# Optimization experiments

Measured on AMD Instinct MI355X. Metric: run time of the kernel, lower is better.

Reference implementation:

```python
import jax, jax.numpy as jnp
import numpy as np

NUM_HEADS = 16
ROPE_BASE = 10000.0
LN_EPS = 1e-5


def _rope_tables(seq_len, head_dim, dtype):
    # half-dim angle table: (seq_len, head_dim//2)
    inv_freq = 1.0 / (ROPE_BASE ** (jnp.arange(0, head_dim, 2, dtype=jnp.float32) / head_dim))
    angles = jnp.arange(seq_len, dtype=jnp.float32)[:, None] * inv_freq[None, :]
    return jnp.cos(angles).astype(dtype), jnp.sin(angles).astype(dtype)


def _apply_rope(x, cos, sin):
    # x: (B, H, S, D_h); rotate interleaved (even, odd) dim pairs
    xe = x[..., 0::2]
    xo = x[..., 1::2]
    c = cos[None, None, :, :]
    s = sin[None, None, :, :]
    re = xe * c - xo * s
    ro = xe * s + xo * c
    return jnp.stack([re, ro], axis=-1).reshape(x.shape)


def _layernorm(x, g, b):
    mu = jnp.mean(x, axis=-1, keepdims=True)
    var = jnp.var(x, axis=-1, keepdims=True)
    return (x - mu) * jax.lax.rsqrt(var + LN_EPS) * g + b


def setup_inputs() -> dict:
    key = jax.random.key(0)
    ks = jax.random.split(key, 8)
    B, S, D, F = 2, 2048, 1024, 4096
    sd = lambda fan_in: 1.0 / np.sqrt(fan_in)
    return {
        "x": jax.random.normal(ks[0], (B, S, D), jnp.float32),
        "in_proj_w": jax.random.normal(ks[1], (3 * D, D), jnp.float32) * sd(D),
        "in_proj_b": jnp.zeros((3 * D,), jnp.float32),
        "out_w": jax.random.normal(ks[2], (D, D), jnp.float32) * sd(D),
        "out_b": jnp.zeros((D,), jnp.float32),
        "w1": jax.random.normal(ks[3], (F, D), jnp.float32) * sd(D),
        "b1": jnp.zeros((F,), jnp.float32),
        "w2": jax.random.normal(ks[4], (D, F), jnp.float32) * sd(F),
        "b2": jnp.zeros((D,), jnp.float32),
        "ln1_g": jnp.ones((D,), jnp.float32),
        "ln1_b": jnp.zeros((D,), jnp.float32),
        "ln2_g": jnp.ones((D,), jnp.float32),
        "ln2_b": jnp.zeros((D,), jnp.float32),
    }


def reference(x, in_proj_w, in_proj_b, out_w, out_b, w1, b1, w2, b2,
              ln1_g, ln1_b, ln2_g, ln2_b):
    B, S, D = x.shape
    H = NUM_HEADS
    Dh = D // H
    scale = Dh ** -0.5

    # fused QKV projection
    qkv = x @ in_proj_w.T + in_proj_b  # (B, S, 3D)
    q, k, v = jnp.split(qkv, 3, axis=-1)
    q = q.reshape(B, S, H, Dh).transpose(0, 2, 1, 3)
    k = k.reshape(B, S, H, Dh).transpose(0, 2, 1, 3)
    v = v.reshape(B, S, H, Dh).transpose(0, 2, 1, 3)

    cos, sin = _rope_tables(S, Dh, x.dtype)
    q = _apply_rope(q, cos, sin)
    k = _apply_rope(k, cos, sin)

    # SDPA (no mask, no dropout)
    scores = jnp.einsum('bhqd,bhkd->bhqk', q, k) * scale
    probs = jax.nn.softmax(scores, axis=-1)
    attn = jnp.einsum('bhqk,bhkd->bhqd', probs, v)
    attn = attn.transpose(0, 2, 1, 3).reshape(B, S, D)
    attn_out = attn @ out_w.T + out_b

    # post-norm encoder layer: residual + LN, FFN, residual + LN
    h = _layernorm(x + attn_out, ln1_g, ln1_b)
    ff = jax.nn.relu(h @ w1.T + b1) @ w2.T + b2
    return _layernorm(h + ff, ln2_g, ln2_b)
```

## Files before the change

### kernel.cpp

```cpp
#include <hip/hip_runtime.h>
#include <math.h>

typedef unsigned short u16;
typedef unsigned int u32;
typedef __attribute__((ext_vector_type(8))) __bf16 bf16x8;
typedef __attribute__((ext_vector_type(4))) float f32x4;

#define AS1 __attribute__((address_space(1)))
#define AS3 __attribute__((address_space(3)))

#define B_ 2
#define S_ 2048
#define D_ 1024
#define H_ 16
#define DH_ 64
#define F_ 4096
#define M_ 4096

__device__ __forceinline__ u16 f2b(float f) {
  u32 u = __builtin_bit_cast(u32, f);
  u += 0x7fffu + ((u >> 16) & 1u);
  return (u16)(u >> 16);
}

__global__ __launch_bounds__(256) void cvt_kernel(const float* __restrict__ in,
                                                  u16* __restrict__ out, int n4) {
  int i = blockIdx.x * 256 + threadIdx.x;
  if (i < n4) {
    float4 v = ((const float4*)in)[i];
    ushort4 o;
    o.x = f2b(v.x); o.y = f2b(v.y); o.z = f2b(v.z); o.w = f2b(v.w);
    ((ushort4*)out)[i] = o;
  }
}

__global__ __launch_bounds__(256) void tables_kernel(float* __restrict__ cosT,
                                                     float* __restrict__ sinT) {
  int idx = blockIdx.x * 256 + threadIdx.x;
  int s = idx >> 5, i = idx & 31;
  float inv = powf(10000.0f, -(float)i / 32.0f);
  float ang = (float)s * inv;
  cosT[idx] = cosf(ang);
  sinT[idx] = sinf(ang);
}

template <bool BIAS, bool RELU, bool RESID, typename OutT>
__global__ __launch_bounds__(256) void gemm_bt(const u16* __restrict__ A,
                                               const u16* __restrict__ Bm,
                                               const float* __restrict__ bias,
                                               const float* __restrict__ resid,
                                               OutT* __restrict__ C, int M, int N, int K) {
  __shared__ u16 sA[128 * 32];
  __shared__ u16 sB[128 * 32];
  const int t = threadIdx.x;
  const int w = t >> 6, lane = t & 63;
  const int fr = lane & 15, fg = lane >> 4;
  const int row0 = blockIdx.y * 128, col0 = blockIdx.x * 128;
  const int wr = (w >> 1) * 64, wc = (w & 1) * 64;

  f32x4 acc[4][4] = {};

  const int rA = t >> 2;
  const int cB = (t & 3) * 16;
  const char* aRead = (const char*)sA + (((wr + fr) * 32 + fg * 8) << 1);
  const char* bRead = (const char*)sB + (((wc + fr) * 32 + fg * 8) << 1);

  for (int k0 = 0; k0 < K; k0 += 32) {
#pragma unroll
    for (int i = 0; i < 2; ++i) {
      const char* srcA = (const char*)(A + (size_t)(row0 + i * 64 + rA) * K + k0) + cB;
      const char* srcB = (const char*)(Bm + (size_t)(col0 + i * 64 + rA) * K + k0) + cB;
      char* dA = (char*)sA + i * 4096 + w * 1024;
      char* dB = (char*)sB + i * 4096 + w * 1024;
      __builtin_amdgcn_global_load_lds((const AS1 u32*)srcA, (AS3 u32*)dA, 16, 0, 0);
      __builtin_amdgcn_global_load_lds((const AS1 u32*)srcB, (AS3 u32*)dB, 16, 0, 0);
    }
    __syncthreads();

    bf16x8 af[4], bfr[4];
#pragma unroll
    for (int m = 0; m < 4; ++m) af[m] = *(const bf16x8*)(aRead + m * 1024);
#pragma unroll
    for (int n = 0; n < 4; ++n) bfr[n] = *(const bf16x8*)(bRead + n * 1024);
#pragma unroll
    for (int m = 0; m < 4; ++m)
#pragma unroll
      for (int n = 0; n < 4; ++n)
        acc[m][n] = __builtin_amdgcn_mfma_f32_16x16x32_bf16(af[m], bfr[n], acc[m][n], 0, 0, 0);
    __syncthreads();
  }

#pragma unroll
  for (int m = 0; m < 4; ++m) {
    const int rowb = row0 + wr + m * 16 + fg * 4;
#pragma unroll
    for (int n = 0; n < 4; ++n) {
      const int col = col0 + wc + n * 16 + fr;
      float bv = BIAS ? bias[col] : 0.0f;
      f32x4 c = acc[m][n];
#pragma unroll
      for (int r = 0; r < 4; ++r) {
        float v = c[r] + bv;
        if (RESID) v += resid[(size_t)(rowb + r) * N + col];
        if (RELU) v = fmaxf(v, 0.0f);
        if constexpr (sizeof(OutT) == 2)
          ((u16*)C)[(size_t)(rowb + r) * N + col] = f2b(v);
        else
          ((float*)C)[(size_t)(rowb + r) * N + col] = v;
      }
    }
  }
}

__global__ __launch_bounds__(256) void rope_kernel(const float* __restrict__ qkv,
                                                   const float* __restrict__ cosT,
                                                   const float* __restrict__ sinT,
                                                   u16* __restrict__ qr, u16* __restrict__ kr,
                                                   u16* __restrict__ vt) {
  const int bh = blockIdx.x;
  const int b = bh >> 4, h = bh & 15;
  const int s0 = blockIdx.y * 64;
  const int t = threadIdx.x;

#pragma unroll
  for (int part = 0; part < 2; ++part) {
    const float* src = qkv + (size_t)(b * S_ + s0) * (3 * D_) + part * D_ + h * DH_;
    u16* dst = (part ? kr : qr) + ((size_t)bh * S_ + s0) * DH_;
    for (int it = 0; it < 8; ++it) {
      int item = it * 256 + t;
      int sl = item >> 5, i = item & 31;
      float2 x2 = *(const float2*)(src + (size_t)sl * (3 * D_) + 2 * i);
      int s = s0 + sl;
      float c = cosT[s * 32 + i], sn = sinT[s * 32 + i];
      float re = x2.x * c - x2.y * sn;
      float ro = x2.x * sn + x2.y * c;
      u32 packed = (u32)f2b(re) | ((u32)f2b(ro) << 16);
      *(u32*)(dst + (size_t)sl * DH_ + 2 * i) = packed;
    }
  }

  __shared__ float tile[64][65];
  const float* vsrc = qkv + (size_t)(b * S_ + s0) * (3 * D_) + 2 * D_ + h * DH_;
  for (int it = 0; it < 16; ++it) {
    int sl = it * 4 + (t >> 6), dh = t & 63;
    tile[sl][dh] = vsrc[(size_t)sl * (3 * D_) + dh];
  }
  __syncthreads();
  u16* vdst = vt + (size_t)bh * DH_ * S_ + s0;
  for (int it = 0; it < 16; ++it) {
    int dh = it * 4 + (t >> 6), sl = t & 63;
    vdst[(size_t)dh * S_ + sl] = f2b(tile[sl][dh]);
  }
}

__global__ __launch_bounds__(256) void attn_kernel(const u16* __restrict__ qr,
                                                   const u16* __restrict__ kr,
                                                   const u16* __restrict__ vt,
                                                   u16* __restrict__ attn) {
  __shared__ u16 sK[2][64 * 64];
  __shared__ u16 sV[2][64 * 64];
  __shared__ u16 plds[4][1024];
  const int bh = blockIdx.x;
  const int b = bh >> 4, h = bh & 15;
  const int q0 = blockIdx.y * 64;
  const int t = threadIdx.x, w = t >> 6, lane = t & 63;
  const int fr = lane & 15, fg = lane >> 4;

  const int qrow = q0 + w * 16 + fr;
  const u16* qbase = qr + ((size_t)bh * S_ + qrow) * DH_;
  bf16x8 qf0 = *(const bf16x8*)(qbase + fg * 8);
  bf16x8 qf1 = *(const bf16x8*)(qbase + 32 + fg * 8);

  const char* kByte = (const char*)(kr + (size_t)bh * S_ * DH_);
  const char* vByte = (const char*)(vt + (size_t)bh * DH_ * S_);
  char* pbase = (char*)&plds[w][0];
  const int ci0 = w * 64 + lane;

  f32x4 oacc[4] = {};
  float m_run = -1e30f, l_run = 0.0f;
  const float lscale = 0.125f * 1.44269504088896340736f;

  auto stage = [&](int bufb, int kt) {
#pragma unroll
    for (int i = 0; i < 2; ++i) {
      int ci = i * 256 + ci0;
      int r = ci >> 3, j = ci & 7;
      int jj = j ^ (r & 7);
      const char* srcK = kByte + (size_t)(kt + r) * 128 + (jj << 4);
      const char* srcV = vByte + (size_t)r * (S_ * 2) + (size_t)kt * 2 + (jj << 4);
      char* dK = (char*)&sK[bufb][0] + i * 4096 + w * 1024;
      char* dV = (char*)&sV[bufb][0] + i * 4096 + w * 1024;
      __builtin_amdgcn_global_load_lds((const AS1 u32*)srcK, (AS3 u32*)dK, 16, 0, 0);
      __builtin_amdgcn_global_load_lds((const AS1 u32*)srcV, (AS3 u32*)dV, 16, 0, 0);
    }
  };

  stage(0, 0);
  __syncthreads();

  int buf = 0;
  for (int kt = 0; kt < S_; kt += 64) {
    if (kt + 64 < S_) stage(buf ^ 1, kt + 64);

    const char* kB = (const char*)&sK[buf][0];
    const char* vB = (const char*)&sV[buf][0];

    f32x4 st[4];
#pragma unroll
    for (int ks = 0; ks < 4; ++ks) {
      const char* rowp = kB + (ks * 16 + fr) * 128;
      bf16x8 kf0 = *(const bf16x8*)(rowp + ((fg ^ (fr & 7)) << 4));
      bf16x8 kf1 = *(const bf16x8*)(rowp + (((fg + 4) ^ (fr & 7)) << 4));
      f32x4 z = {};
      z = __builtin_amdgcn_mfma_f32_16x16x32_bf16(kf0, qf0, z, 0, 0, 0);
      st[ks] = __builtin_amdgcn_mfma_f32_16x16x32_bf16(kf1, qf1, z, 0, 0, 0);
    }

    float pm = -1e30f;
#pragma unroll
    for (int ks = 0; ks < 4; ++ks) {
      st[ks] *= lscale;
#pragma unroll
      for (int r = 0; r < 4; ++r) pm = fmaxf(pm, st[ks][r]);
    }
    pm = fmaxf(pm, __shfl_xor(pm, 16));
    pm = fmaxf(pm, __shfl_xor(pm, 32));
    float mnew = fmaxf(m_run, pm);
    float alpha = __builtin_amdgcn_exp2f(m_run - mnew);
    float psum = 0.0f;
#pragma unroll
    for (int ks = 0; ks < 4; ++ks) {
      float p0 = __builtin_amdgcn_exp2f(st[ks][0] - mnew);
      float p1 = __builtin_amdgcn_exp2f(st[ks][1] - mnew);
      float p2 = __builtin_amdgcn_exp2f(st[ks][2] - mnew);
      float p3 = __builtin_amdgcn_exp2f(st[ks][3] - mnew);
      psum += (p0 + p1) + (p2 + p3);
      u32 lo = (u32)f2b(p0) | ((u32)f2b(p1) << 16);
      u32 hi = (u32)f2b(p2) | ((u32)f2b(p3) << 16);
      int wb = fr * 128 + (((ks * 32) | (fg * 8)) ^ ((fr & 7) << 4));
      *(uint2*)(pbase + wb) = make_uint2(lo, hi);
    }
    psum += __shfl_xor(psum, 16);
    psum += __shfl_xor(psum, 32);
    l_run = l_run * alpha + psum;
    m_run = mnew;
#pragma unroll
    for (int d = 0; d < 4; ++d) oacc[d] *= alpha;

    asm volatile("s_waitcnt lgkmcnt(0)" ::: "memory");
    __builtin_amdgcn_sched_barrier(0);

#pragma unroll
    for (int ksub = 0; ksub < 2; ++ksub) {
      int rb = fr * 128 + (((ksub * 64) | (fg * 16)) ^ ((fr & 7) << 4));
      bf16x8 pf = *(const bf16x8*)(pbase + rb);
#pragma unroll
      for (int d = 0; d < 4; ++d) {
        const char* vp = vB + (d * 16 + fr) * 128 + ((((ksub * 4) | fg) ^ (fr & 7)) << 4);
        bf16x8 vf = *(const bf16x8*)vp;
        oacc[d] = __builtin_amdgcn_mfma_f32_16x16x32_bf16(vf, pf, oacc[d], 0, 0, 0);
      }
    }
    __syncthreads();
    buf ^= 1;
  }

  const float inv_l = 1.0f / l_run;
  u16* obase = attn + (size_t)(b * S_ + q0 + w * 16 + fr) * D_ + h * DH_;
#pragma unroll
  for (int d = 0; d < 4; ++d) {
    ushort4 o4;
    o4.x = f2b(oacc[d][0] * inv_l);
    o4.y = f2b(oacc[d][1] * inv_l);
    o4.z = f2b(oacc[d][2] * inv_l);
    o4.w = f2b(oacc[d][3] * inv_l);
    *(ushort4*)(obase + d * 16 + fg * 4) = o4;
  }
}

template <bool WRITE_BF16>
__global__ __launch_bounds__(256) void ln_kernel(const float* __restrict__ in,
                                                 const float* __restrict__ gamma,
                                                 const float* __restrict__ beta,
                                                 float* __restrict__ outf,
                                                 u16* __restrict__ outb) {
  const int row = blockIdx.x;
  const int t = threadIdx.x;
  const float4 v = ((const float4*)(in + (size_t)row * D_))[t];
  float s = v.x + v.y + v.z + v.w;
  float ss = v.x * v.x + v.y * v.y + v.z * v.z + v.w * v.w;
#pragma unroll
  for (int off = 1; off < 64; off <<= 1) {
    s += __shfl_xor(s, off);
    ss += __shfl_xor(ss, off);
  }
  __shared__ float red[8];
  const int w = t >> 6, lane = t & 63;
  if (lane == 0) { red[w] = s; red[4 + w] = ss; }
  __syncthreads();
  s = red[0] + red[1] + red[2] + red[3];
  ss = red[4] + red[5] + red[6] + red[7];
  const float mu = s * (1.0f / D_);
  const float var = ss * (1.0f / D_) - mu * mu;
  const float rstd = rsqrtf(var + 1e-5f);
  const float4 g4 = ((const float4*)gamma)[t];
  const float4 b4 = ((const float4*)beta)[t];
  float4 o;
  o.x = (v.x - mu) * rstd * g4.x + b4.x;
  o.y = (v.y - mu) * rstd * g4.y + b4.y;
  o.z = (v.z - mu) * rstd * g4.z + b4.z;
  o.w = (v.w - mu) * rstd * g4.w + b4.w;
  ((float4*)(outf + (size_t)row * D_))[t] = o;
  if constexpr (WRITE_BF16) {
    ushort4 ob;
    ob.x = f2b(o.x); ob.y = f2b(o.y); ob.z = f2b(o.z); ob.w = f2b(o.w);
    ((ushort4*)(outb + (size_t)row * D_))[t] = ob;
  }
}

extern "C" void kernel_launch(void* const* d_in, const int* in_sizes, int n_in,
                              void* d_out, int out_size, void* d_ws, size_t ws_size,
                              hipStream_t stream) {
  const float* x = (const float*)d_in[0];
  const float* in_proj_w = (const float*)d_in[1];
  const float* in_proj_b = (const float*)d_in[2];
  const float* out_w = (const float*)d_in[3];
  const float* out_b = (const float*)d_in[4];
  const float* w1 = (const float*)d_in[5];
  const float* b1 = (const float*)d_in[6];
  const float* w2 = (const float*)d_in[7];
  const float* b2 = (const float*)d_in[8];
  const float* ln1_g = (const float*)d_in[9];
  const float* ln1_b = (const float*)d_in[10];
  const float* ln2_g = (const float*)d_in[11];
  const float* ln2_b = (const float*)d_in[12];

  char* ws = (char*)d_ws;
  u16* wib = (u16*)(ws + 0);
  u16* wob = (u16*)(ws + 6291456);
  u16* w1b = (u16*)(ws + 8388608);
  u16* w2b = (u16*)(ws + 16777216);
  float* cosT = (float*)(ws + 25165824);
  float* sinT = (float*)(ws + 25427968);
  float* qkv = (float*)(ws + 25690112);
  u16* ff = (u16*)(ws + 25690112);
  float* preln2 = (float*)(ws + 59244544);
  u16* xb = (u16*)(ws + 76021760);
  u16* attnb = (u16*)(ws + 76021760);
  u16* qrb = (u16*)(ws + 84410368);
  u16* krb = (u16*)(ws + 92798976);
  float* preln1 = (float*)(ws + 84410368);
  u16* vtb = (u16*)(ws + 101187584);
  u16* hb = (u16*)(ws + 101187584);
  float* hf = (float*)(ws + 109576192);
  (void)ws_size; (void)in_sizes; (void)n_in; (void)out_size;

  cvt_kernel<<<4096, 256, 0, stream>>>(x, xb, 1048576);
  cvt_kernel<<<3072, 256, 0, stream>>>(in_proj_w, wib, 786432);
  cvt_kernel<<<1024, 256, 0, stream>>>(out_w, wob, 262144);
  cvt_kernel<<<4096, 256, 0, stream>>>(w1, w1b, 1048576);
  cvt_kernel<<<4096, 256, 0, stream>>>(w2, w2b, 1048576);
  tables_kernel<<<256, 256, 0, stream>>>(cosT, sinT);

  gemm_bt<true, false, false, float><<<dim3(24, 32), 256, 0, stream>>>(
      xb, wib, in_proj_b, nullptr, qkv, M_, 3 * D_, D_);

  rope_kernel<<<dim3(32, 32), 256, 0, stream>>>(qkv, cosT, sinT, qrb, krb, vtb);

  attn_kernel<<<dim3(32, 32), 256, 0, stream>>>(qrb, krb, vtb, attnb);

  gemm_bt<true, false, true, float><<<dim3(8, 32), 256, 0, stream>>>(
      attnb, wob, out_b, x, preln1, M_, D_, D_);

  ln_kernel<true><<<4096, 256, 0, stream>>>(preln1, ln1_g, ln1_b, hf, hb);

  gemm_bt<true, true, false, u16><<<dim3(32, 32), 256, 0, stream>>>(
      hb, w1b, b1, nullptr, ff, M_, F_, D_);

  gemm_bt<true, false, true, float><<<dim3(8, 32), 256, 0, stream>>>(
      ff, w2b, b2, hf, preln2, M_, D_, F_);

  ln_kernel<false><<<4096, 256, 0, stream>>>(preln2, ln2_g, ln2_b, (float*)d_out, nullptr);
}
```

Before: 445.1 us.

## Split-K narrow GEMMs, fuse bias/residual into LN, swizzle LDS, bf16 QKV output

The N=1024 GEMMs (out-proj and FFN down) now use split-K across two z-slices writing fp32 partials, which doubles the block count from 256 to 512 to fill more CUs. A new reduce_ln kernel sums the partials with bias and residual before layernorm, replacing the separate residual epilogue. The GEMM LDS layout is XOR-swizzled to reduce bank conflicts on fragment reads. The QKV projection now writes bf16 instead of fp32, halving that traffic for the rope kernel. The cost is extra partial-buffer writes and reads, plus a small precision change on QKV.

```diff
diff --git a/kernel.cpp b/kernel.cpp
--- a/kernel.cpp
+++ b/kernel.cpp
@@ -44,12 +44,12 @@
   sinT[idx] = sinf(ang);
 }
 
-template <bool BIAS, bool RELU, bool RESID, typename OutT>
+template <bool BIAS, bool RELU, bool SPLIT, typename OutT>
 __global__ __launch_bounds__(256) void gemm_bt(const u16* __restrict__ A,
                                                const u16* __restrict__ Bm,
                                                const float* __restrict__ bias,
-                                               const float* __restrict__ resid,
-                                               OutT* __restrict__ C, int M, int N, int K) {
+                                               OutT* __restrict__ C, int M, int N, int K,
+                                               int kChunk) {
   __shared__ u16 sA[128 * 32];
   __shared__ u16 sB[128 * 32];
   const int t = threadIdx.x;
@@ -61,15 +61,17 @@
   f32x4 acc[4][4] = {};
 
   const int rA = t >> 2;
-  const int cB = (t & 3) * 16;
-  const char* aRead = (const char*)sA + (((wr + fr) * 32 + fg * 8) << 1);
-  const char* bRead = (const char*)sB + (((wc + fr) * 32 + fg * 8) << 1);
-
-  for (int k0 = 0; k0 < K; k0 += 32) {
+  const int jj = ((t & 3) ^ ((t >> 3) & 3)) << 4;
+  const int rdswz = ((fg ^ ((fr >> 1) & 3)) << 4);
+  const char* aRead = (const char*)sA + (wr + fr) * 64 + rdswz;
+  const char* bRead = (const char*)sB + (wc + fr) * 64 + rdswz;
+
+  const int kb = blockIdx.z * kChunk;
+  for (int k0 = kb; k0 < kb + kChunk; k0 += 32) {
 #pragma unroll
     for (int i = 0; i < 2; ++i) {
-      const char* srcA = (const char*)(A + (size_t)(row0 + i * 64 + rA) * K + k0) + cB;
-      const char* srcB = (const char*)(Bm + (size_t)(col0 + i * 64 + rA) * K + k0) + cB;
+      const char* srcA = (const char*)(A + (size_t)(row0 + i * 64 + rA) * K + k0) + jj;
+      const char* srcB = (const char*)(Bm + (size_t)(col0 + i * 64 + rA) * K + k0) + jj;
       char* dA = (char*)sA + i * 4096 + w * 1024;
       char* dB = (char*)sB + i * 4096 + w * 1024;
       __builtin_amdgcn_global_load_lds((const AS1 u32*)srcA, (AS3 u32*)dA, 16, 0, 0);
@@ -90,6 +92,8 @@
     __syncthreads();
   }
 
+  OutT* Cp = C;
+  if constexpr (SPLIT) Cp = C + (size_t)blockIdx.z * M * N;
 #pragma unroll
   for (int m = 0; m < 4; ++m) {
     const int rowb = row0 + wr + m * 16 + fg * 4;
@@ -101,18 +105,17 @@
 #pragma unroll
       for (int r = 0; r < 4; ++r) {
         float v = c[r] + bv;
-        if (RESID) v += resid[(size_t)(rowb + r) * N + col];
         if (RELU) v = fmaxf(v, 0.0f);
         if constexpr (sizeof(OutT) == 2)
-          ((u16*)C)[(size_t)(rowb + r) * N + col] = f2b(v);
+          ((u16*)Cp)[(size_t)(rowb + r) * N + col] = f2b(v);
         else
-          ((float*)C)[(size_t)(rowb + r) * N + col] = v;
+          ((float*)Cp)[(size_t)(rowb + r) * N + col] = v;
       }
     }
   }
 }
 
-__global__ __launch_bounds__(256) void rope_kernel(const float* __restrict__ qkv,
+__global__ __launch_bounds__(256) void rope_kernel(const u16* __restrict__ qkv,
                                                    const float* __restrict__ cosT,
                                                    const float* __restrict__ sinT,
                                                    u16* __restrict__ qr, u16* __restrict__ kr,
@@ -124,23 +127,25 @@
 
 #pragma unroll
   for (int part = 0; part < 2; ++part) {
-    const float* src = qkv + (size_t)(b * S_ + s0) * (3 * D_) + part * D_ + h * DH_;
+    const u16* src = qkv + (size_t)(b * S_ + s0) * (3 * D_) + part * D_ + h * DH_;
     u16* dst = (part ? kr : qr) + ((size_t)bh * S_ + s0) * DH_;
     for (int it = 0; it < 8; ++it) {
       int item = it * 256 + t;
       int sl = item >> 5, i = item & 31;
-      float2 x2 = *(const float2*)(src + (size_t)sl * (3 * D_) + 2 * i);
+      u32 v = *(const u32*)(src + (size_t)sl * (3 * D_) + 2 * i);
+      float xe = __builtin_bit_cast(float, v << 16);
+      float xo = __builtin_bit_cast(float, v & 0xffff0000u);
       int s = s0 + sl;
       float c = cosT[s * 32 + i], sn = sinT[s * 32 + i];
-      float re = x2.x * c - x2.y * sn;
-      float ro = x2.x * sn + x2.y * c;
+      float re = xe * c - xo * sn;
+      float ro = xe * sn + xo * c;
       u32 packed = (u32)f2b(re) | ((u32)f2b(ro) << 16);
       *(u32*)(dst + (size_t)sl * DH_ + 2 * i) = packed;
     }
   }
 
-  __shared__ float tile[64][65];
-  const float* vsrc = qkv + (size_t)(b * S_ + s0) * (3 * D_) + 2 * D_ + h * DH_;
+  __shared__ u16 tile[64][65];
+  const u16* vsrc = qkv + (size_t)(b * S_ + s0) * (3 * D_) + 2 * D_ + h * DH_;
   for (int it = 0; it < 16; ++it) {
     int sl = it * 4 + (t >> 6), dh = t & 63;
     tile[sl][dh] = vsrc[(size_t)sl * (3 * D_) + dh];
@@ -149,7 +154,7 @@
   u16* vdst = vt + (size_t)bh * DH_ * S_ + s0;
   for (int it = 0; it < 16; ++it) {
     int dh = it * 4 + (t >> 6), sl = t & 63;
-    vdst[(size_t)dh * S_ + sl] = f2b(tile[sl][dh]);
+    vdst[(size_t)dh * S_ + sl] = tile[sl][dh];
   }
 }
 
@@ -278,15 +283,27 @@
   }
 }
 
-template <bool WRITE_BF16>
-__global__ __launch_bounds__(256) void ln_kernel(const float* __restrict__ in,
-                                                 const float* __restrict__ gamma,
-                                                 const float* __restrict__ beta,
-                                                 float* __restrict__ outf,
-                                                 u16* __restrict__ outb) {
+template <int NS, bool WRITE_BF16>
+__global__ __launch_bounds__(256) void reduce_ln_kernel(const float* __restrict__ parts,
+                                                        const float* __restrict__ bias,
+                                                        const float* __restrict__ resid,
+                                                        const float* __restrict__ gamma,
+                                                        const float* __restrict__ beta,
+                                                        float* __restrict__ outf,
+                                                        u16* __restrict__ outb) {
   const int row = blockIdx.x;
   const int t = threadIdx.x;
-  const float4 v = ((const float4*)(in + (size_t)row * D_))[t];
+  const size_t base = (size_t)row * D_;
+  float4 v = ((const float4*)bias)[t];
+  {
+    const float4 r4 = ((const float4*)(resid + base))[t];
+    v.x += r4.x; v.y += r4.y; v.z += r4.z; v.w += r4.w;
+  }
+#pragma unroll
+  for (int s = 0; s < NS; ++s) {
+    const float4 p4 = ((const float4*)(parts + (size_t)s * M_ * D_ + base))[t];
+    v.x += p4.x; v.y += p4.y; v.z += p4.z; v.w += p4.w;
+  }
   float s = v.x + v.y + v.z + v.w;
   float ss = v.x * v.x + v.y * v.y + v.z * v.z + v.w * v.w;
 #pragma unroll
@@ -310,11 +327,11 @@
   o.y = (v.y - mu) * rstd * g4.y + b4.y;
   o.z = (v.z - mu) * rstd * g4.z + b4.z;
   o.w = (v.w - mu) * rstd * g4.w + b4.w;
-  ((float4*)(outf + (size_t)row * D_))[t] = o;
+  ((float4*)(outf + base))[t] = o;
   if constexpr (WRITE_BF16) {
     ushort4 ob;
     ob.x = f2b(o.x); ob.y = f2b(o.y); ob.z = f2b(o.z); ob.w = f2b(o.w);
-    ((ushort4*)(outb + (size_t)row * D_))[t] = ob;
+    ((ushort4*)(outb + base))[t] = ob;
   }
 }
 
@@ -342,17 +359,16 @@
   u16* w2b = (u16*)(ws + 16777216);
   float* cosT = (float*)(ws + 25165824);
   float* sinT = (float*)(ws + 25427968);
-  float* qkv = (float*)(ws + 25690112);
-  u16* ff = (u16*)(ws + 25690112);
-  float* preln2 = (float*)(ws + 59244544);
-  u16* xb = (u16*)(ws + 76021760);
-  u16* attnb = (u16*)(ws + 76021760);
-  u16* qrb = (u16*)(ws + 84410368);
-  u16* krb = (u16*)(ws + 92798976);
-  float* preln1 = (float*)(ws + 84410368);
-  u16* vtb = (u16*)(ws + 101187584);
-  u16* hb = (u16*)(ws + 101187584);
-  float* hf = (float*)(ws + 109576192);
+  u16* qkvb = (u16*)(ws + 25690112);
+  float* part = (float*)(ws + 25690112);
+  u16* qrb = (u16*)(ws + 59244544);
+  u16* krb = (u16*)(ws + 67633152);
+  u16* vtb = (u16*)(ws + 76021760);
+  u16* attnb = (u16*)(ws + 84410368);
+  u16* ff = (u16*)(ws + 59244544);
+  u16* xb = (u16*)(ws + 92798976);
+  float* hf = (float*)(ws + 92798976);
+  u16* hb = (u16*)(ws + 109576192);
   (void)ws_size; (void)in_sizes; (void)n_in; (void)out_size;
 
   cvt_kernel<<<4096, 256, 0, stream>>>(x, xb, 1048576);
@@ -362,23 +378,22 @@
   cvt_kernel<<<4096, 256, 0, stream>>>(w2, w2b, 1048576);
   tables_kernel<<<256, 256, 0, stream>>>(cosT, sinT);
 
-  gemm_bt<true, false, false, float><<<dim3(24, 32), 256, 0, stream>>>(
-      xb, wib, in_proj_b, nullptr, qkv, M_, 3 * D_, D_);
-
-  rope_kernel<<<dim3(32, 32), 256, 0, stream>>>(qkv, cosT, sinT, qrb, krb, vtb);
+  gemm_bt<true, false, false, u16><<<dim3(24, 32), 256, 0, stream>>>(
+      xb, wib, in_proj_b, qkvb, M_, 3 * D_, D_, D_);
+
+  rope_kernel<<<dim3(32, 32), 256, 0, stream>>>(qkvb, cosT, sinT, qrb, krb, vtb);
 
   attn_kernel<<<dim3(32, 32), 256, 0, stream>>>(qrb, krb, vtb, attnb);
 
-  gemm_bt<true, false, true, float><<<dim3(8, 32), 256, 0, stream>>>(
-      attnb, wob, out_b, x, preln1, M_, D_, D_);
-
-  ln_kernel<true><<<4096, 256, 0, stream>>>(preln1, ln1_g, ln1_b, hf, hb);
+  gemm_bt<false, false, true, float><<<dim3(8, 32, 2), 256, 0, stream>>>(
+      attnb, wob, nullptr, part, M_, D_, D_, 512);
+  reduce_ln_kernel<2, true><<<4096, 256, 0, stream>>>(part, out_b, x, ln1_g, ln1_b, hf, hb);
 
   gemm_bt<true, true, false, u16><<<dim3(32, 32), 256, 0, stream>>>(
-      hb, w1b, b1, nullptr, ff, M_, F_, D_);
-
-  gemm_bt<true, false, true, float><<<dim3(8, 32), 256, 0, stream>>>(
-      ff, w2b, b2, hf, preln2, M_, D_, F_);
-
-  ln_kernel<false><<<4096, 256, 0, stream>>>(preln2, ln2_g, ln2_b, (float*)d_out, nullptr);
-}
+      hb, w1b, b1, ff, M_, F_, D_, D_);
+
+  gemm_bt<false, false, true, float><<<dim3(8, 32, 2), 256, 0, stream>>>(
+      ff, w2b, nullptr, part, M_, D_, F_, 2048);
+  reduce_ln_kernel<2, false><<<4096, 256, 0, stream>>>(part, b2, hf, ln2_g, ln2_b,
+                                                       (float*)d_out, nullptr);
+}
```

Result: faster. 412.1 us (-7.4%).
